# Optimization experiments

Measured on AMD Instinct MI355X. Metric: run time of the kernel, lower is better.

## Reference

```python
import jax, jax.numpy as jnp
import numpy as np

BITS = 4            # OPU.bits
VEC = 64            # OPU.input_vector_len / weight_vector_len
QMAX = 2 ** (BITS - 1) - 1   # 7


def ste_round(x):
    # straight-through round (onn_round)
    return x + jax.lax.stop_gradient(jnp.round(x) - x)


@jax.custom_vjp
def onn_dot_sum(x, w):
    # x: [N, R, VEC], w: [VEC, R, M]
    # per-chunk matmul -> clamp to int8 range -> binarize (>=0 -> 1) -> sum over chunks
    s = jnp.einsum('nrc,crm->nrm', x, w)
    s = jnp.clip(s, -128.0, 127.0)
    return jnp.where(s < 0, 0.0, 1.0).sum(axis=1)  # [N, M]


def _onn_dot_fwd(x, w):
    return onn_dot_sum(x, w), (x, w)


def _onn_dot_bwd(res, g):
    # onn_dot_fun.backward: straight-through past clamp+threshold;
    # each chunk receives the same grad g (sum over chunks).
    x, w = res
    gx = jnp.einsum('nm,crm->nrc', g, w)
    gw = jnp.einsum('nrc,nm->crm', x, g)
    return gx, gw


onn_dot_sum.defvjp(_onn_dot_fwd, _onn_dot_bwd)


def _onn_conv2d(inp, weight):
    B, C, H, W = inp.shape
    Cout, Cin, k, _ = weight.shape
    pad = (k - 1) // 2  # SAME, stride=1
    # im2col (matches torch F.unfold channel-major ordering: C, kh, kw)
    xp = jnp.pad(inp, ((0, 0), (0, 0), (pad, pad), (pad, pad)))
    patches = jnp.stack([xp[:, :, i:i + H, j:j + W]
                         for i in range(k) for j in range(k)], axis=2)  # [B,C,k*k,H,W]
    inp_unf = patches.reshape(B, C * k * k, H * W).transpose(0, 2, 1)    # [B,L,D]
    # weight quantization: STE round + clamp to 4-bit signed range
    scale = (2 ** BITS - 1) / (weight.max() - weight.min() + 1e-9)
    wq = jnp.clip(ste_round(weight * scale), -QMAX, QMAX)
    w_ = wq.reshape(Cout, -1).T                                          # [D, Cout]
    D = C * k * k
    repeats = -(-D // VEC)
    padD = VEC * repeats - D
    x = jnp.pad(inp_unf, ((0, 0), (0, 0), (0, padD))).reshape(B * H * W, repeats, VEC)
    wpad = jnp.pad(w_, ((0, padD), (0, 0)))                              # [VEC*R, Cout]
    wr = wpad.T.reshape(Cout, repeats, VEC).transpose(2, 1, 0)           # [VEC,R,Cout]
    temp = onn_dot_sum(x, wr)                                            # [B*L, Cout]
    return temp.reshape(B, H * W, Cout).transpose(0, 2, 1).reshape(B, Cout, H, W)


def setup_inputs() -> dict:
    key = jax.random.key(0)
    k1, k2 = jax.random.split(key)
    B, Cin, H, W = 16, 128, 32, 32
    Cout, k = 256, 3
    inp = jax.random.normal(k1, (B, Cin, H, W), dtype=jnp.float32)
    fan_in = Cin * k * k
    bound = 1.0 / np.sqrt(fan_in)  # kaiming_uniform with a=sqrt(5)
    weight = jax.random.uniform(k2, (Cout, Cin, k, k), dtype=jnp.float32,
                                minval=-bound, maxval=bound)
    return {"inp": inp, "weight": weight}


def reference(inp, weight):
    return _onn_conv2d(inp, weight)
```

## Files before the change

### kernel.cpp

```cpp
#include <hip/hip_runtime.h>


#define TAU 0.03f
#define HITCAP 2048

typedef short short8 __attribute__((ext_vector_type(8)));
typedef float f32x4 __attribute__((ext_vector_type(4)));
typedef unsigned int uv4 __attribute__((ext_vector_type(4)));

__device__ __forceinline__ unsigned short bf16rn(float v) {
    unsigned u = __float_as_uint(v);
    unsigned r = u + 0x7fffu + ((u >> 16) & 1u);
    return (unsigned short)(r >> 16);
}

__global__ __launch_bounds__(256) void k_prep(const float* __restrict__ w,
                                              const float* __restrict__ inp,
                                              float* __restrict__ pmin,
                                              float* __restrict__ pmax,
                                              unsigned* __restrict__ xpk) {
    if (blockIdx.x < 64) {
        int tid = blockIdx.x * 256 + threadIdx.x;
        float vmin = 1e30f, vmax = -1e30f;
        for (int i = tid; i < 294912; i += 64 * 256) {
            float v = w[i];
            vmin = fminf(vmin, v);
            vmax = fmaxf(vmax, v);
        }
        #pragma unroll
        for (int off = 32; off > 0; off >>= 1) {
            vmin = fminf(vmin, __shfl_down(vmin, off, 64));
            vmax = fmaxf(vmax, __shfl_down(vmax, off, 64));
        }
        __shared__ float smin[4], smax[4];
        int wave = threadIdx.x >> 6;
        if ((threadIdx.x & 63) == 0) { smin[wave] = vmin; smax[wave] = vmax; }
        __syncthreads();
        if (threadIdx.x == 0) {
            #pragma unroll
            for (int i = 1; i < 4; i++) {
                vmin = fminf(vmin, smin[i]);
                vmax = fmaxf(vmax, smax[i]);
            }
            pmin[blockIdx.x] = vmin;
            pmax[blockIdx.x] = vmax;
        }
    } else {
        int bc = blockIdx.x - 64;
        const float* src = inp + (size_t)bc * 1024;
        unsigned* dst = xpk + (size_t)bc * 1156;
        #pragma unroll
        for (int i = 0; i < 5; ++i) {
            int idx = threadIdx.x + i * 256;
            if (idx < 1156) {
                int yy = idx / 34, xx = idx - yy * 34;
                float v = 0.0f;
                int ys = yy - 1, xs_ = xx - 1;
                if ((unsigned)ys < 32u && (unsigned)xs_ < 32u) v = src[ys * 32 + xs_];
                unsigned short h = bf16rn(v);
                float hf = __uint_as_float((unsigned)h << 16);
                unsigned short l = bf16rn(v - hf);
                dst[idx] = (unsigned)h | ((unsigned)l << 16);
            }
        }
    }
}

__device__ __forceinline__ float block_scale(const float* pmin, const float* pmax,
                                             float* sca_lds) {
    int t = threadIdx.x;
    if (t < 64) {
        float vmin = pmin[t];
        float vmax = pmax[t];
        #pragma unroll
        for (int off = 32; off > 0; off >>= 1) {
            vmin = fminf(vmin, __shfl_down(vmin, off, 64));
            vmax = fmaxf(vmax, __shfl_down(vmax, off, 64));
        }
        if (t == 0) {
            float tt = __fadd_rn(__fsub_rn(vmax, vmin), 1e-9f);
            *sca_lds = __fdiv_rn(15.0f, tt);
        }
    }
    __syncthreads();
    return *sca_lds;
}

__global__ __launch_bounds__(256) void k_quantb(const float* __restrict__ w,
                                                const float* __restrict__ pmin,
                                                const float* __restrict__ pmax,
                                                uv4* __restrict__ wqb) {
    __shared__ float sca;
    float s = block_scale(pmin, pmax, &sca);
    int slot = blockIdx.x * 256 + threadIdx.x;
    int lane = slot & 63;
    int sub = slot >> 6;
    int khalf = sub & 1;
    int mt = (sub >> 1) & 3;
    int gr = sub >> 3;
    int g = gr / 18, r = gr - g * 18;
    int m = g * 64 + mt * 16 + (lane & 15);
    int dbase = r * 64 + khalf * 32 + (lane >> 4) * 8;
    const float* wp = w + (size_t)m * 1152 + dbase;
    unsigned o[4];
    #pragma unroll
    for (int p = 0; p < 4; ++p) {
        float q0 = rintf(__fmul_rn(wp[2 * p], s));
        float q1 = rintf(__fmul_rn(wp[2 * p + 1], s));
        q0 = fminf(fmaxf(q0, -7.0f), 7.0f);
        q1 = fminf(fmaxf(q1, -7.0f), 7.0f);
        o[p] = (unsigned)bf16rn(q0) | ((unsigned)bf16rn(q1) << 16);
    }
    uv4 v; v.x = o[0]; v.y = o[1]; v.z = o[2]; v.w = o[3];
    wqb[slot] = v;
}

#define XLD(o) (*reinterpret_cast<const unsigned*>(xpkB + (xdelta + (unsigned)(o))))

#define ISSUE_B(rr, dst) do {                                                  \
    const int4* _oa = reinterpret_cast<const int4*>(&ofs_s[(rr) * 64 + quad * 8]); \
    int4 _o0 = _oa[0], _o1 = _oa[1];                                           \
    const int4* _ob = reinterpret_cast<const int4*>(&ofs_s[(rr) * 64 + 32 + quad * 8]); \
    int4 _o2 = _ob[0], _o3 = _ob[1];                                           \
    dst[0] = XLD(_o0.x); dst[1] = XLD(_o0.y); dst[2] = XLD(_o0.z); dst[3] = XLD(_o0.w); \
    dst[4] = XLD(_o1.x); dst[5] = XLD(_o1.y); dst[6] = XLD(_o1.z); dst[7] = XLD(_o1.w); \
    dst[8] = XLD(_o2.x); dst[9] = XLD(_o2.y); dst[10] = XLD(_o2.z); dst[11] = XLD(_o2.w); \
    dst[12] = XLD(_o3.x); dst[13] = XLD(_o3.y); dst[14] = XLD(_o3.z); dst[15] = XLD(_o3.w); \
} while (0)

#define AIDX(rr, mm) ((((mm) >> 2) * 9216) + (rr) * 512 + (((mm) & 3) * 128))

__global__ __launch_bounds__(512, 4) void k_main(const unsigned* __restrict__ xpk,
                                                 const uv4* __restrict__ wqb,
                                                 const float* __restrict__ inp,
                                                 const float* __restrict__ weight,
                                                 const float* __restrict__ pmin,
                                                 const float* __restrict__ pmax,
                                                 float* __restrict__ out) {
    __shared__ alignas(16) int ofs_s[1152];
    __shared__ unsigned hitbuf[HITCAP];
    __shared__ unsigned red_s[4][64][9];
    __shared__ unsigned hitcnt;
    __shared__ float sca;

    const int t = threadIdx.x;
    if (t == 0) hitcnt = 0u;
    float sc = block_scale(pmin, pmax, &sca);
    for (int k = t; k < 1152; k += 512) {
        int cin = k / 9;
        int rem = k - cin * 9;
        int kh = rem / 3;
        int kw = rem - kh * 3;
        ofs_s[k] = (cin * 1156 + kh * 34 + kw) * 4;
    }
    __syncthreads();

    const int lane = t & 63;
    const int wv8 = t >> 6;
    const int nt = wv8 >> 1;
    const int kz = wv8 & 1;
    const int quad = lane >> 4;
    const int nl = lane & 15;
    const int n0 = blockIdx.x * 64;
    const int g = blockIdx.y;
    const int b = n0 >> 10;
    const int r0 = kz * 9, rend = r0 + 9;

    const int sy_w = ((n0 & 1023) >> 5) + (nt >> 1);
    const int col0 = (nt & 1) * 16;
    const char* __restrict__ xpkB = (const char*)xpk;
    const unsigned xdelta =
        ((unsigned)b * (128u * 1156u) + (unsigned)(sy_w * 34 + col0 + nl)) * 4u;
    const uv4* __restrict__ aw = wqb + (size_t)g * (2 * 18 * 512) + lane;

    unsigned negpk[8][2] = {};
    unsigned long long hitacc = 0ull;

    unsigned pb[16];
    ISSUE_B(r0, pb);
    short8 ac0 = __builtin_bit_cast(short8, aw[AIDX(r0, 0)]);
    short8 ac1 = __builtin_bit_cast(short8, aw[AIDX(r0, 0) + 64]);

    for (int r = r0; r < rend; ++r) {
        short8 bhi[2], blo[2];
        #pragma unroll
        for (int kh2 = 0; kh2 < 2; ++kh2) {
            union { unsigned d[4]; short8 v; } H, L;
            #pragma unroll
            for (int p = 0; p < 4; ++p) {
                unsigned ua = pb[kh2 * 8 + 2 * p], ub = pb[kh2 * 8 + 2 * p + 1];
                H.d[p] = __builtin_amdgcn_perm(ub, ua, 0x05040100u);
                L.d[p] = __builtin_amdgcn_perm(ub, ua, 0x07060302u);
            }
            bhi[kh2] = H.v;
            blo[kh2] = L.v;
        }

        const int rn = (r + 1 < rend) ? r + 1 : r;
        ISSUE_B(rn, pb);

        f32x4 accs[8];
        #pragma unroll
        for (int mt = 0; mt < 8; ++mt) {
            const int pn = (mt == 7) ? AIDX(rn, 0) : AIDX(r, mt + 1);
            short8 an0 = __builtin_bit_cast(short8, aw[pn]);
            short8 an1 = __builtin_bit_cast(short8, aw[pn + 64]);

            f32x4 acc = {0.0f, 0.0f, 0.0f, 0.0f};
            acc = __builtin_amdgcn_mfma_f32_16x16x32_bf16(ac0, bhi[0], acc, 0, 0, 0);
            acc = __builtin_amdgcn_mfma_f32_16x16x32_bf16(ac1, bhi[1], acc, 0, 0, 0);
            acc = __builtin_amdgcn_mfma_f32_16x16x32_bf16(ac0, blo[0], acc, 0, 0, 0);
            acc = __builtin_amdgcn_mfma_f32_16x16x32_bf16(ac1, blo[1], acc, 0, 0, 0);
            accs[mt] = acc;
            #pragma unroll
            for (int p = 0; p < 2; ++p) {
                unsigned sb0 = __float_as_uint(acc[2 * p]) >> 31;
                unsigned sb1 = __float_as_uint(acc[2 * p + 1]) >> 31;
                negpk[mt][p] += sb0 + (sb1 << 16);
                hitacc |= __ballot(__builtin_fabsf(acc[2 * p]) < TAU);
                hitacc |= __ballot(__builtin_fabsf(acc[2 * p + 1]) < TAU);
            }
            ac0 = an0;
            ac1 = an1;
        }

        if (hitacc) {
            #pragma unroll
            for (int mt = 0; mt < 8; ++mt)
                #pragma unroll
                for (int i = 0; i < 4; ++i) {
                    float s = accs[mt][i];
                    if (__builtin_fabsf(s) < TAU) {
                        unsigned ge = (__float_as_uint(s) >> 31) ^ 1u;
                        unsigned idx = atomicAdd(&hitcnt, 1u);
                        if (idx < (unsigned)HITCAP) {
                            unsigned m = (unsigned)(g * 128 + mt * 16 + quad * 4 + i);
                            unsigned n = (unsigned)(n0 + nt * 16 + nl);
                            hitbuf[idx] = n | ((unsigned)r << 14) | (m << 19)
                                            | (ge << 27);
                        }
                    }
                }
            hitacc = 0ull;
        }
    }

    if (kz == 1) {
        #pragma unroll
        for (int mt = 0; mt < 8; ++mt) {
            unsigned c0 = negpk[mt][0] & 0xffffu, c1 = negpk[mt][0] >> 16;
            unsigned c2 = negpk[mt][1] & 0xffffu, c3 = negpk[mt][1] >> 16;
            red_s[nt][lane][mt] = c0 | (c1 << 8) | (c2 << 16) | (c3 << 24);
        }
    }
    __syncthreads();
    if (kz == 0) {
        const int n = n0 + nt * 16 + nl;
        const int p = n & 1023;
        #pragma unroll
        for (int mt = 0; mt < 8; ++mt) {
            unsigned pk = red_s[nt][lane][mt];
            unsigned tot0 = (negpk[mt][0] & 0xffffu) + (pk & 255u);
            unsigned tot1 = (negpk[mt][0] >> 16) + ((pk >> 8) & 255u);
            unsigned tot2 = (negpk[mt][1] & 0xffffu) + ((pk >> 16) & 255u);
            unsigned tot3 = (negpk[mt][1] >> 16) + (pk >> 24);
            int mb = g * 128 + mt * 16 + quad * 4;
            size_t obase = ((size_t)(b * 256 + mb)) << 10;
            out[obase + p]              = (float)(18u - tot0);
            out[obase + (1ull << 10) + p] = (float)(18u - tot1);
            out[obase + (2ull << 10) + p] = (float)(18u - tot2);
            out[obase + (3ull << 10) + p] = (float)(18u - tot3);
        }
    }

    __syncthreads();
    unsigned tot = hitcnt;
    if (tot > (unsigned)HITCAP) tot = (unsigned)HITCAP;
    for (unsigned i = t; i < tot; i += 512) {
        unsigned u = hitbuf[i];
        int n = u & 16383;
        int r = (u >> 14) & 31;
        int m = (u >> 19) & 255;
        int bit = (u >> 27) & 1;
        int bb = n >> 10, p = n & 1023, y = p >> 5, x = p & 31;
        const float* ib = inp + (size_t)bb * (128 * 32 * 32);
        const float* wp = weight + (size_t)m * 1152;
        float s = 0.0f;
        int d = r * 64;
        for (int c = 0; c < 64; ++c, ++d) {
            int ci = d / 9, rem = d - ci * 9;
            int kh = rem / 3, kw = rem - kh * 3;
            int yy = y + kh - 1, xx = x + kw - 1;
            float xv = 0.0f;
            if ((unsigned)yy < 32u && (unsigned)xx < 32u)
                xv = ib[(ci * 32 + yy) * 32 + xx];
            float q = rintf(__fmul_rn(wp[d], sc));
            q = fminf(fmaxf(q, -7.0f), 7.0f);
            s = __fadd_rn(s, __fmul_rn(xv, q));
        }
        int nb = (s >= 0.0f) ? 1 : 0;
        if (nb != bit)
            atomicAdd(&out[(((size_t)(bb * 256 + m)) << 10) + p], nb ? 1.0f : -1.0f);
    }
}

extern "C" void kernel_launch(void* const* d_in, const int* in_sizes, int n_in,
                              void* d_out, int out_size, void* d_ws, size_t ws_size,
                              hipStream_t stream) {
    const float* inp    = (const float*)d_in[0];
    const float* weight = (const float*)d_in[1];
    float* out = (float*)d_out;

    char* ws = (char*)d_ws;
    float*    pmin  = (float*)(ws + 0);
    float*    pmax  = (float*)(ws + 256);
    uv4*      wqb   = (uv4*)(ws + 1024);
    unsigned* xpk   = (unsigned*)(ws + 590848);

    k_prep<<<2112, 256, 0, stream>>>(weight, inp, pmin, pmax, xpk);
    k_quantb<<<144, 256, 0, stream>>>(weight, pmin, pmax, wqb);

    dim3 grid(256, 2);
    k_main<<<grid, 512, 0, stream>>>(xpk, wqb, inp, weight, pmin, pmax, out);
}
```

Before: 119.3 us.

## Deepen weight-fragment prefetch to four tiles and swizzle block-to-tile mapping

Replaces the one-tile-ahead prefetch of A (weight) fragments with a four-register-set rotation, so each weight load is issued four MFMA groups before it is used. This hides more global-load latency behind matrix work. Blocks are also remapped from a linear launch index with a stride-8 swizzle, so neighbouring blocks get different n-tiles and output groups, which is meant to change cache locality and XCD distribution. The deeper prefetch holds more VGPRs live, which risks spills or lower occupancy under the 512x4 launch bounds.

```diff
diff --git a/kernel.cpp b/kernel.cpp
--- a/kernel.cpp
+++ b/kernel.cpp
@@ -130,6 +130,25 @@
 
 #define AIDX(rr, mm) ((((mm) >> 2) * 9216) + (rr) * 512 + (((mm) & 3) * 128))
 
+#define MT_STEP(mt, sA, sB, pr, pm) do {                                        \
+    f32x4 acc = {0.0f, 0.0f, 0.0f, 0.0f};                                       \
+    acc = __builtin_amdgcn_mfma_f32_16x16x32_bf16(sA, bhi[0], acc, 0, 0, 0);    \
+    acc = __builtin_amdgcn_mfma_f32_16x16x32_bf16(sB, bhi[1], acc, 0, 0, 0);    \
+    acc = __builtin_amdgcn_mfma_f32_16x16x32_bf16(sA, blo[0], acc, 0, 0, 0);    \
+    acc = __builtin_amdgcn_mfma_f32_16x16x32_bf16(sB, blo[1], acc, 0, 0, 0);    \
+    sA = __builtin_bit_cast(short8, aw[AIDX(pr, pm)]);                          \
+    sB = __builtin_bit_cast(short8, aw[AIDX(pr, pm) + 64]);                     \
+    accs[mt] = acc;                                                             \
+    _Pragma("unroll")                                                           \
+    for (int p = 0; p < 2; ++p) {                                               \
+        unsigned sb0 = __float_as_uint(acc[2 * p]) >> 31;                       \
+        unsigned sb1 = __float_as_uint(acc[2 * p + 1]) >> 31;                   \
+        negpk[mt][p] += sb0 + (sb1 << 16);                                      \
+        hitacc |= __ballot(__builtin_fabsf(acc[2 * p]) < TAU);                  \
+        hitacc |= __ballot(__builtin_fabsf(acc[2 * p + 1]) < TAU);              \
+    }                                                                           \
+} while (0)
+
 __global__ __launch_bounds__(512, 4) void k_main(const unsigned* __restrict__ xpk,
                                                  const uv4* __restrict__ wqb,
                                                  const float* __restrict__ inp,
@@ -155,14 +174,17 @@
     }
     __syncthreads();
 
+    const int lin = (int)(blockIdx.y * gridDim.x + blockIdx.x);
+    const int nlin = (lin & 7) * 64 + (lin >> 3);
+    const int g = nlin >> 8;
+    const int n0 = (nlin & 255) * 64;
+
     const int lane = t & 63;
     const int wv8 = t >> 6;
     const int nt = wv8 >> 1;
     const int kz = wv8 & 1;
     const int quad = lane >> 4;
     const int nl = lane & 15;
-    const int n0 = blockIdx.x * 64;
-    const int g = blockIdx.y;
     const int b = n0 >> 10;
     const int r0 = kz * 9, rend = r0 + 9;
 
@@ -178,8 +200,14 @@
 
     unsigned pb[16];
     ISSUE_B(r0, pb);
-    short8 ac0 = __builtin_bit_cast(short8, aw[AIDX(r0, 0)]);
-    short8 ac1 = __builtin_bit_cast(short8, aw[AIDX(r0, 0) + 64]);
+    short8 a0A = __builtin_bit_cast(short8, aw[AIDX(r0, 0)]);
+    short8 a0B = __builtin_bit_cast(short8, aw[AIDX(r0, 0) + 64]);
+    short8 a1A = __builtin_bit_cast(short8, aw[AIDX(r0, 1)]);
+    short8 a1B = __builtin_bit_cast(short8, aw[AIDX(r0, 1) + 64]);
+    short8 a2A = __builtin_bit_cast(short8, aw[AIDX(r0, 2)]);
+    short8 a2B = __builtin_bit_cast(short8, aw[AIDX(r0, 2) + 64]);
+    short8 a3A = __builtin_bit_cast(short8, aw[AIDX(r0, 3)]);
+    short8 a3B = __builtin_bit_cast(short8, aw[AIDX(r0, 3) + 64]);
 
     for (int r = r0; r < rend; ++r) {
         short8 bhi[2], blo[2];
@@ -200,29 +228,14 @@
         ISSUE_B(rn, pb);
 
         f32x4 accs[8];
-        #pragma unroll
-        for (int mt = 0; mt < 8; ++mt) {
-            const int pn = (mt == 7) ? AIDX(rn, 0) : AIDX(r, mt + 1);
-            short8 an0 = __builtin_bit_cast(short8, aw[pn]);
-            short8 an1 = __builtin_bit_cast(short8, aw[pn + 64]);
-
-            f32x4 acc = {0.0f, 0.0f, 0.0f, 0.0f};
-            acc = __builtin_amdgcn_mfma_f32_16x16x32_bf16(ac0, bhi[0], acc, 0, 0, 0);
-            acc = __builtin_amdgcn_mfma_f32_16x16x32_bf16(ac1, bhi[1], acc, 0, 0, 0);
-            acc = __builtin_amdgcn_mfma_f32_16x16x32_bf16(ac0, blo[0], acc, 0, 0, 0);
-            acc = __builtin_amdgcn_mfma_f32_16x16x32_bf16(ac1, blo[1], acc, 0, 0, 0);
-            accs[mt] = acc;
-            #pragma unroll
-            for (int p = 0; p < 2; ++p) {
-                unsigned sb0 = __float_as_uint(acc[2 * p]) >> 31;
-                unsigned sb1 = __float_as_uint(acc[2 * p + 1]) >> 31;
-                negpk[mt][p] += sb0 + (sb1 << 16);
-                hitacc |= __ballot(__builtin_fabsf(acc[2 * p]) < TAU);
-                hitacc |= __ballot(__builtin_fabsf(acc[2 * p + 1]) < TAU);
-            }
-            ac0 = an0;
-            ac1 = an1;
-        }
+        MT_STEP(0, a0A, a0B, r, 4);
+        MT_STEP(1, a1A, a1B, r, 5);
+        MT_STEP(2, a2A, a2B, r, 6);
+        MT_STEP(3, a3A, a3B, r, 7);
+        MT_STEP(4, a0A, a0B, rn, 0);
+        MT_STEP(5, a1A, a1B, rn, 1);
+        MT_STEP(6, a2A, a2B, rn, 2);
+        MT_STEP(7, a3A, a3B, rn, 3);
 
         if (hitacc) {
             #pragma unroll
@@ -266,7 +279,7 @@
             unsigned tot3 = (negpk[mt][1] >> 16) + (pk >> 24);
             int mb = g * 128 + mt * 16 + quad * 4;
             size_t obase = ((size_t)(b * 256 + mb)) << 10;
-            out[obase + p]              = (float)(18u - tot0);
+            out[obase + p]                = (float)(18u - tot0);
             out[obase + (1ull << 10) + p] = (float)(18u - tot1);
             out[obase + (2ull << 10) + p] = (float)(18u - tot2);
             out[obase + (3ull << 10) + p] = (float)(18u - tot3);
```

New measurement: 123.4 us. +3.4%, slower.

## Switch main GEMM to int8 MFMA with fixed-point split activations and prebuilt im2col

Applied to the files above, without the earlier changes.

Activations are quantized to fixed point (scale 2048) and split into hi/lo int8 halves, and the 4-bit weights are stored as int8, so the main loop uses i32 16x16x64 int8 MFMAs instead of the bf16 hi/lo decomposition. A separate k_bmat kernel materializes the im2col B-fragments in global memory, which replaces the per-lane gather through LDS offsets. The near-zero fallback threshold becomes an integer band, and the block order is swizzled for L2 locality. The cost is an extra ~37MB workspace write/read and quantization of the inputs, which relies on the exact-recompute path to correct sign flips near zero.

```diff
diff --git a/kernel.cpp b/kernel.cpp
--- a/kernel.cpp
+++ b/kernel.cpp
@@ -1,68 +1,39 @@
 #include <hip/hip_runtime.h>
 
 
-#define TAU 0.03f
-#define HITCAP 2048
-
-typedef short short8 __attribute__((ext_vector_type(8)));
-typedef float f32x4 __attribute__((ext_vector_type(4)));
+#define THRI 123
+#define HITCAP 1024
+
 typedef unsigned int uv4 __attribute__((ext_vector_type(4)));
-
-__device__ __forceinline__ unsigned short bf16rn(float v) {
-    unsigned u = __float_as_uint(v);
-    unsigned r = u + 0x7fffu + ((u >> 16) & 1u);
-    return (unsigned short)(r >> 16);
-}
+typedef int iv4 __attribute__((ext_vector_type(4)));
 
 __global__ __launch_bounds__(256) void k_prep(const float* __restrict__ w,
-                                              const float* __restrict__ inp,
                                               float* __restrict__ pmin,
-                                              float* __restrict__ pmax,
-                                              unsigned* __restrict__ xpk) {
-    if (blockIdx.x < 64) {
-        int tid = blockIdx.x * 256 + threadIdx.x;
-        float vmin = 1e30f, vmax = -1e30f;
-        for (int i = tid; i < 294912; i += 64 * 256) {
-            float v = w[i];
-            vmin = fminf(vmin, v);
-            vmax = fmaxf(vmax, v);
-        }
-        #pragma unroll
-        for (int off = 32; off > 0; off >>= 1) {
-            vmin = fminf(vmin, __shfl_down(vmin, off, 64));
-            vmax = fmaxf(vmax, __shfl_down(vmax, off, 64));
-        }
-        __shared__ float smin[4], smax[4];
-        int wave = threadIdx.x >> 6;
-        if ((threadIdx.x & 63) == 0) { smin[wave] = vmin; smax[wave] = vmax; }
-        __syncthreads();
-        if (threadIdx.x == 0) {
-            #pragma unroll
-            for (int i = 1; i < 4; i++) {
-                vmin = fminf(vmin, smin[i]);
-                vmax = fmaxf(vmax, smax[i]);
-            }
-            pmin[blockIdx.x] = vmin;
-            pmax[blockIdx.x] = vmax;
-        }
-    } else {
-        int bc = blockIdx.x - 64;
-        const float* src = inp + (size_t)bc * 1024;
-        unsigned* dst = xpk + (size_t)bc * 1156;
-        #pragma unroll
-        for (int i = 0; i < 5; ++i) {
-            int idx = threadIdx.x + i * 256;
-            if (idx < 1156) {
-                int yy = idx / 34, xx = idx - yy * 34;
-                float v = 0.0f;
-                int ys = yy - 1, xs_ = xx - 1;
-                if ((unsigned)ys < 32u && (unsigned)xs_ < 32u) v = src[ys * 32 + xs_];
-                unsigned short h = bf16rn(v);
-                float hf = __uint_as_float((unsigned)h << 16);
-                unsigned short l = bf16rn(v - hf);
-                dst[idx] = (unsigned)h | ((unsigned)l << 16);
-            }
-        }
+                                              float* __restrict__ pmax) {
+    int tid = blockIdx.x * 256 + threadIdx.x;
+    float vmin = 1e30f, vmax = -1e30f;
+    for (int i = tid; i < 294912; i += 64 * 256) {
+        float v = w[i];
+        vmin = fminf(vmin, v);
+        vmax = fmaxf(vmax, v);
+    }
+    #pragma unroll
+    for (int off = 32; off > 0; off >>= 1) {
+        vmin = fminf(vmin, __shfl_down(vmin, off, 64));
+        vmax = fmaxf(vmax, __shfl_down(vmax, off, 64));
+    }
+    __shared__ float smin[4], smax[4];
+    int wave = threadIdx.x >> 6;
+    if ((threadIdx.x & 63) == 0) { smin[wave] = vmin; smax[wave] = vmax; }
+    __syncthreads();
+    if (threadIdx.x == 0) {
+        #pragma unroll
+        for (int i = 1; i < 4; i++) {
+            vmin = fminf(vmin, smin[i]);
+            vmax = fmaxf(vmax, smax[i]);
+        }
+        pmin[blockIdx.x] = vmin;
+        pmax[blockIdx.x] = vmax;
     }
 }
 
@@ -86,58 +57,73 @@
     return *sca_lds;
 }
 
+__global__ __launch_bounds__(256) void k_bmat(const float* __restrict__ inp,
+                                              uv4* __restrict__ bmh,
+                                              uv4* __restrict__ bml) {
+    const int t = threadIdx.x;
+    const int lane = t & 63;
+    const int unit = blockIdx.x * 4 + (t >> 6);
+    const int r = unit >> 10;
+    const int n16 = unit & 1023;
+    const int nl = lane & 15, kq = lane >> 4;
+    const int n = n16 * 16 + nl;
+    const int b = n >> 10, p = n & 1023, y = p >> 5, x = p & 31;
+    const float* ib = inp + ((size_t)b << 17);
+    unsigned hw[4] = {0u, 0u, 0u, 0u}, lw[4] = {0u, 0u, 0u, 0u};
+    #pragma unroll
+    for (int j = 0; j < 16; ++j) {
+        int d = r * 64 + kq * 16 + j;
+        int ci = d / 9, rem = d - ci * 9;
+        int kh = rem / 3, kw = rem - kh * 3;
+        int yy = y + kh - 1, xx = x + kw - 1;
+        float v = 0.0f;
+        if ((unsigned)yy < 32u && (unsigned)xx < 32u)
+            v = ib[(ci << 10) + yy * 32 + xx];
+        int xq = (int)rintf(v * 2048.0f);
+        int hi = (xq + 64) >> 7;
+        int lo = xq - (hi << 7);
+        hw[j >> 2] |= ((unsigned)hi & 255u) << ((j & 3) * 8);
+        lw[j >> 2] |= ((unsigned)lo & 255u) << ((j & 3) * 8);
+    }
+    int slot = unit * 64 + lane;
+    uv4 hv; hv.x = hw[0]; hv.y = hw[1]; hv.z = hw[2]; hv.w = hw[3];
+    uv4 lv; lv.x = lw[0]; lv.y = lw[1]; lv.z = lw[2]; lv.w = lw[3];
+    bmh[slot] = hv;
+    bml[slot] = lv;
+}
+
 __global__ __launch_bounds__(256) void k_quantb(const float* __restrict__ w,
                                                 const float* __restrict__ pmin,
                                                 const float* __restrict__ pmax,
-                                                uv4* __restrict__ wqb) {
+                                                uv4* __restrict__ aq) {
     __shared__ float sca;
     float s = block_scale(pmin, pmax, &sca);
     int slot = blockIdx.x * 256 + threadIdx.x;
     int lane = slot & 63;
     int sub = slot >> 6;
-    int khalf = sub & 1;
-    int mt = (sub >> 1) & 3;
-    int gr = sub >> 3;
-    int g = gr / 18, r = gr - g * 18;
-    int m = g * 64 + mt * 16 + (lane & 15);
-    int dbase = r * 64 + khalf * 32 + (lane >> 4) * 8;
+    int mtg = sub & 15, r = sub >> 4;
+    int m = mtg * 16 + (lane & 15);
+    int dbase = r * 64 + (lane >> 4) * 16;
     const float* wp = w + (size_t)m * 1152 + dbase;
-    unsigned o[4];
+    unsigned wv_[4] = {0u, 0u, 0u, 0u};
     #pragma unroll
-    for (int p = 0; p < 4; ++p) {
-        float q0 = rintf(__fmul_rn(wp[2 * p], s));
-        float q1 = rintf(__fmul_rn(wp[2 * p + 1], s));
-        q0 = fminf(fmaxf(q0, -7.0f), 7.0f);
-        q1 = fminf(fmaxf(q1, -7.0f), 7.0f);
-        o[p] = (unsigned)bf16rn(q0) | ((unsigned)bf16rn(q1) << 16);
-    }
-    uv4 v; v.x = o[0]; v.y = o[1]; v.z = o[2]; v.w = o[3];
-    wqb[slot] = v;
-}
-
-#define XLD(o) (*reinterpret_cast<const unsigned*>(xpkB + (xdelta + (unsigned)(o))))
-
-#define ISSUE_B(rr, dst) do {                                                  \
-    const int4* _oa = reinterpret_cast<const int4*>(&ofs_s[(rr) * 64 + quad * 8]); \
-    int4 _o0 = _oa[0], _o1 = _oa[1];                                           \
-    const int4* _ob = reinterpret_cast<const int4*>(&ofs_s[(rr) * 64 + 32 + quad * 8]); \
-    int4 _o2 = _ob[0], _o3 = _ob[1];                                           \
-    dst[0] = XLD(_o0.x); dst[1] = XLD(_o0.y); dst[2] = XLD(_o0.z); dst[3] = XLD(_o0.w); \
-    dst[4] = XLD(_o1.x); dst[5] = XLD(_o1.y); dst[6] = XLD(_o1.z); dst[7] = XLD(_o1.w); \
-    dst[8] = XLD(_o2.x); dst[9] = XLD(_o2.y); dst[10] = XLD(_o2.z); dst[11] = XLD(_o2.w); \
-    dst[12] = XLD(_o3.x); dst[13] = XLD(_o3.y); dst[14] = XLD(_o3.z); dst[15] = XLD(_o3.w); \
-} while (0)
-
-#define AIDX(rr, mm) ((((mm) >> 2) * 9216) + (rr) * 512 + (((mm) & 3) * 128))
-
-__global__ __launch_bounds__(512, 4) void k_main(const unsigned* __restrict__ xpk,
-                                                 const uv4* __restrict__ wqb,
+    for (int j = 0; j < 16; ++j) {
+        float q = rintf(__fmul_rn(wp[j], s));
+        q = fminf(fmaxf(q, -7.0f), 7.0f);
+        wv_[j >> 2] |= ((unsigned)(int)q & 255u) << ((j & 3) * 8);
+    }
+    uv4 v; v.x = wv_[0]; v.y = wv_[1]; v.z = wv_[2]; v.w = wv_[3];
+    aq[slot] = v;
+}
+
+__global__ __launch_bounds__(512, 4) void k_main(const uv4* __restrict__ aq,
+                                                 const uv4* __restrict__ bmh,
+                                                 const uv4* __restrict__ bml,
                                                  const float* __restrict__ inp,
                                                  const float* __restrict__ weight,
                                                  const float* __restrict__ pmin,
                                                  const float* __restrict__ pmax,
                                                  float* __restrict__ out) {
-    __shared__ alignas(16) int ofs_s[1152];
     __shared__ unsigned hitbuf[HITCAP];
     __shared__ unsigned red_s[4][64][9];
     __shared__ unsigned hitcnt;
@@ -146,14 +132,11 @@
     const int t = threadIdx.x;
     if (t == 0) hitcnt = 0u;
     float sc = block_scale(pmin, pmax, &sca);
-    for (int k = t; k < 1152; k += 512) {
-        int cin = k / 9;
-        int rem = k - cin * 9;
-        int kh = rem / 3;
-        int kw = rem - kh * 3;
-        ofs_s[k] = (cin * 1156 + kh * 34 + kw) * 4;
-    }
-    __syncthreads();
+
+    const int lin = (int)(blockIdx.y * gridDim.x + blockIdx.x);
+    const int nlin = (lin & 7) * 64 + (lin >> 3);
+    const int g = nlin >> 8;
+    const int n0 = (nlin & 255) * 64;
 
     const int lane = t & 63;
     const int wv8 = t >> 6;
@@ -161,67 +144,46 @@
     const int kz = wv8 & 1;
     const int quad = lane >> 4;
     const int nl = lane & 15;
-    const int n0 = blockIdx.x * 64;
-    const int g = blockIdx.y;
     const int b = n0 >> 10;
     const int r0 = kz * 9, rend = r0 + 9;
 
-    const int sy_w = ((n0 & 1023) >> 5) + (nt >> 1);
-    const int col0 = (nt & 1) * 16;
-    const char* __restrict__ xpkB = (const char*)xpk;
-    const unsigned xdelta =
-        ((unsigned)b * (128u * 1156u) + (unsigned)(sy_w * 34 + col0 + nl)) * 4u;
-    const uv4* __restrict__ aw = wqb + (size_t)g * (2 * 18 * 512) + lane;
+    const int n16g = (n0 >> 4) + nt;
+    const int sb = n16g * 64 + lane;
+    const uv4* __restrict__ awq = aq + lane;
 
     unsigned negpk[8][2] = {};
     unsigned long long hitacc = 0ull;
 
-    unsigned pb[16];
-    ISSUE_B(r0, pb);
-    short8 ac0 = __builtin_bit_cast(short8, aw[AIDX(r0, 0)]);
-    short8 ac1 = __builtin_bit_cast(short8, aw[AIDX(r0, 0) + 64]);
+    uv4 pbh = bmh[r0 * 65536 + sb];
+    uv4 pbl = bml[r0 * 65536 + sb];
 
     for (int r = r0; r < rend; ++r) {
-        short8 bhi[2], blo[2];
-        #pragma unroll
-        for (int kh2 = 0; kh2 < 2; ++kh2) {
-            union { unsigned d[4]; short8 v; } H, L;
+        iv4 bhv = __builtin_bit_cast(iv4, pbh);
+        iv4 blv = __builtin_bit_cast(iv4, pbl);
+
+        const int rn = (r + 1 < rend) ? r + 1 : r;
+        pbh = bmh[rn * 65536 + sb];
+        pbl = bml[rn * 65536 + sb];
+
+        iv4 accs[8];
+        #pragma unroll
+        for (int mt = 0; mt < 8; ++mt) {
+            iv4 av = __builtin_bit_cast(iv4, awq[(r * 16 + g * 8 + mt) * 64]);
+            iv4 z = {0, 0, 0, 0};
+            iv4 ah = __builtin_amdgcn_mfma_i32_16x16x64_i8(av, bhv, z, 0, 0, 0);
+            iv4 al = __builtin_amdgcn_mfma_i32_16x16x64_i8(av, blv, z, 0, 0, 0);
+            iv4 s;
             #pragma unroll
-            for (int p = 0; p < 4; ++p) {
-                unsigned ua = pb[kh2 * 8 + 2 * p], ub = pb[kh2 * 8 + 2 * p + 1];
-                H.d[p] = __builtin_amdgcn_perm(ub, ua, 0x05040100u);
-                L.d[p] = __builtin_amdgcn_perm(ub, ua, 0x07060302u);
-            }
-            bhi[kh2] = H.v;
-            blo[kh2] = L.v;
-        }
-
-        const int rn = (r + 1 < rend) ? r + 1 : r;
-        ISSUE_B(rn, pb);
-
-        f32x4 accs[8];
-        #pragma unroll
-        for (int mt = 0; mt < 8; ++mt) {
-            const int pn = (mt == 7) ? AIDX(rn, 0) : AIDX(r, mt + 1);
-            short8 an0 = __builtin_bit_cast(short8, aw[pn]);
-            short8 an1 = __builtin_bit_cast(short8, aw[pn + 64]);
-
-            f32x4 acc = {0.0f, 0.0f, 0.0f, 0.0f};
-            acc = __builtin_amdgcn_mfma_f32_16x16x32_bf16(ac0, bhi[0], acc, 0, 0, 0);
-            acc = __builtin_amdgcn_mfma_f32_16x16x32_bf16(ac1, bhi[1], acc, 0, 0, 0);
-            acc = __builtin_amdgcn_mfma_f32_16x16x32_bf16(ac0, blo[0], acc, 0, 0, 0);
-            acc = __builtin_amdgcn_mfma_f32_16x16x32_bf16(ac1, blo[1], acc, 0, 0, 0);
-            accs[mt] = acc;
+            for (int i = 0; i < 4; ++i) s[i] = (ah[i] << 7) + al[i];
+            accs[mt] = s;
             #pragma unroll
             for (int p = 0; p < 2; ++p) {
-                unsigned sb0 = __float_as_uint(acc[2 * p]) >> 31;
-                unsigned sb1 = __float_as_uint(acc[2 * p + 1]) >> 31;
+                unsigned sb0 = (unsigned)s[2 * p] >> 31;
+                unsigned sb1 = (unsigned)s[2 * p + 1] >> 31;
                 negpk[mt][p] += sb0 + (sb1 << 16);
-                hitacc |= __ballot(__builtin_fabsf(acc[2 * p]) < TAU);
-                hitacc |= __ballot(__builtin_fabsf(acc[2 * p + 1]) < TAU);
+                hitacc |= __ballot((unsigned)(s[2 * p] + (THRI - 1)) < (unsigned)(2 * THRI - 1));
+                hitacc |= __ballot((unsigned)(s[2 * p + 1] + (THRI - 1)) < (unsigned)(2 * THRI - 1));
             }
-            ac0 = an0;
-            ac1 = an1;
         }
 
         if (hitacc) {
@@ -229,9 +191,9 @@
             for (int mt = 0; mt < 8; ++mt)
                 #pragma unroll
                 for (int i = 0; i < 4; ++i) {
-                    float s = accs[mt][i];
-                    if (__builtin_fabsf(s) < TAU) {
-                        unsigned ge = (__float_as_uint(s) >> 31) ^ 1u;
+                    int s = accs[mt][i];
+                    if ((unsigned)(s + (THRI - 1)) < (unsigned)(2 * THRI - 1)) {
+                        unsigned ge = ((unsigned)s >> 31) ^ 1u;
                         unsigned idx = atomicAdd(&hitcnt, 1u);
                         if (idx < (unsigned)HITCAP) {
                             unsigned m = (unsigned)(g * 128 + mt * 16 + quad * 4 + i);
@@ -266,7 +228,7 @@
             unsigned tot3 = (negpk[mt][1] >> 16) + (pk >> 24);
             int mb = g * 128 + mt * 16 + quad * 4;
             size_t obase = ((size_t)(b * 256 + mb)) << 10;
-            out[obase + p]              = (float)(18u - tot0);
+            out[obase + p]                = (float)(18u - tot0);
             out[obase + (1ull << 10) + p] = (float)(18u - tot1);
             out[obase + (2ull << 10) + p] = (float)(18u - tot2);
             out[obase + (3ull << 10) + p] = (float)(18u - tot3);
@@ -312,14 +274,16 @@
     float* out = (float*)d_out;
 
     char* ws = (char*)d_ws;
-    float*    pmin  = (float*)(ws + 0);
-    float*    pmax  = (float*)(ws + 256);
-    uv4*      wqb   = (uv4*)(ws + 1024);
-    unsigned* xpk   = (unsigned*)(ws + 590848);
-
-    k_prep<<<2112, 256, 0, stream>>>(weight, inp, pmin, pmax, xpk);
-    k_quantb<<<144, 256, 0, stream>>>(weight, pmin, pmax, wqb);
+    float* pmin = (float*)(ws + 0);
+    float* pmax = (float*)(ws + 256);
+    uv4*   aq   = (uv4*)(ws + 1024);
+    uv4*   bmh  = (uv4*)(ws + 296960);
+    uv4*   bml  = (uv4*)(ws + 19171328);
+
+    k_prep<<<64, 256, 0, stream>>>(weight, pmin, pmax);
+    k_bmat<<<4608, 256, 0, stream>>>(inp, bmh, bml);
+    k_quantb<<<72, 256, 0, stream>>>(weight, pmin, pmax, aq);
 
     dim3 grid(256, 2);
-    k_main<<<grid, 512, 0, stream>>>(xpk, wqb, inp, weight, pmin, pmax, out);
-}
+    k_main<<<grid, 512, 0, stream>>>(aq, bmh, bml, inp, weight, pmin, pmax, out);
+}
```

New measurement: 148.9 us. 24.8% more time.

## Fuse weight min/max and quantization into prep kernel; swizzle main grid

Applied to the files above, without the earlier changes.

Merges the weight min/max reduction and the weight quantization into the input-packing kernel, so one launch replaces two. Each of the 144 quantization blocks now recomputes the full weight min/max itself with float4 loads, which removes the partial-reduction buffers. The main kernel reads a single precomputed scale instead of reducing 64 partials in every block. It also remaps block indices so that consecutive blocks interleave across both output-channel groups and spatial tiles. The cost is redundant reading of the whole weight tensor by every quantization block.

```diff
diff --git a/kernel.cpp b/kernel.cpp
--- a/kernel.cpp
+++ b/kernel.cpp
@@ -16,42 +16,17 @@
 
 __global__ __launch_bounds__(256) void k_prep(const float* __restrict__ w,
                                               const float* __restrict__ inp,
-                                              float* __restrict__ pmin,
-                                              float* __restrict__ pmax,
-                                              unsigned* __restrict__ xpk) {
-    if (blockIdx.x < 64) {
-        int tid = blockIdx.x * 256 + threadIdx.x;
-        float vmin = 1e30f, vmax = -1e30f;
-        for (int i = tid; i < 294912; i += 64 * 256) {
-            float v = w[i];
-            vmin = fminf(vmin, v);
-            vmax = fmaxf(vmax, v);
-        }
-        #pragma unroll
-        for (int off = 32; off > 0; off >>= 1) {
-            vmin = fminf(vmin, __shfl_down(vmin, off, 64));
-            vmax = fmaxf(vmax, __shfl_down(vmax, off, 64));
-        }
-        __shared__ float smin[4], smax[4];
-        int wave = threadIdx.x >> 6;
-        if ((threadIdx.x & 63) == 0) { smin[wave] = vmin; smax[wave] = vmax; }
-        __syncthreads();
-        if (threadIdx.x == 0) {
-            #pragma unroll
-            for (int i = 1; i < 4; i++) {
-                vmin = fminf(vmin, smin[i]);
-                vmax = fmaxf(vmax, smax[i]);
-            }
-            pmin[blockIdx.x] = vmin;
-            pmax[blockIdx.x] = vmax;
-        }
-    } else {
-        int bc = blockIdx.x - 64;
+                                              unsigned* __restrict__ xpk,
+                                              uv4* __restrict__ wqb,
+                                              float* __restrict__ wsscale) {
+    const int t = threadIdx.x;
+    if (blockIdx.x < 2048) {
+        int bc = blockIdx.x;
         const float* src = inp + (size_t)bc * 1024;
         unsigned* dst = xpk + (size_t)bc * 1156;
         #pragma unroll
         for (int i = 0; i < 5; ++i) {
-            int idx = threadIdx.x + i * 256;
+            int idx = t + i * 256;
             if (idx < 1156) {
                 int yy = idx / 34, xx = idx - yy * 34;
                 float v = 0.0f;
@@ -63,56 +38,59 @@
                 dst[idx] = (unsigned)h | ((unsigned)l << 16);
             }
         }
-    }
-}
-
-__device__ __forceinline__ float block_scale(const float* pmin, const float* pmax,
-                                             float* sca_lds) {
-    int t = threadIdx.x;
-    if (t < 64) {
-        float vmin = pmin[t];
-        float vmax = pmax[t];
+    } else {
+        const float4* w4 = (const float4*)w;
+        float vmin = 1e30f, vmax = -1e30f;
+        for (int i = t; i < 73728; i += 256) {
+            float4 v = w4[i];
+            vmin = fminf(vmin, fminf(fminf(v.x, v.y), fminf(v.z, v.w)));
+            vmax = fmaxf(vmax, fmaxf(fmaxf(v.x, v.y), fmaxf(v.z, v.w)));
+        }
         #pragma unroll
         for (int off = 32; off > 0; off >>= 1) {
             vmin = fminf(vmin, __shfl_down(vmin, off, 64));
             vmax = fmaxf(vmax, __shfl_down(vmax, off, 64));
         }
+        __shared__ float smin[4], smax[4];
+        __shared__ float sca;
+        int wave = t >> 6;
+        if ((t & 63) == 0) { smin[wave] = vmin; smax[wave] = vmax; }
+        __syncthreads();
         if (t == 0) {
+            #pragma unroll
+            for (int i = 1; i < 4; i++) {
+                vmin = fminf(vmin, smin[i]);
+                vmax = fmaxf(vmax, smax[i]);
+            }
             float tt = __fadd_rn(__fsub_rn(vmax, vmin), 1e-9f);
-            *sca_lds = __fdiv_rn(15.0f, tt);
-        }
-    }
-    __syncthreads();
-    return *sca_lds;
-}
-
-__global__ __launch_bounds__(256) void k_quantb(const float* __restrict__ w,
-                                                const float* __restrict__ pmin,
-                                                const float* __restrict__ pmax,
-                                                uv4* __restrict__ wqb) {
-    __shared__ float sca;
-    float s = block_scale(pmin, pmax, &sca);
-    int slot = blockIdx.x * 256 + threadIdx.x;
-    int lane = slot & 63;
-    int sub = slot >> 6;
-    int khalf = sub & 1;
-    int mt = (sub >> 1) & 3;
-    int gr = sub >> 3;
-    int g = gr / 18, r = gr - g * 18;
-    int m = g * 64 + mt * 16 + (lane & 15);
-    int dbase = r * 64 + khalf * 32 + (lane >> 4) * 8;
-    const float* wp = w + (size_t)m * 1152 + dbase;
-    unsigned o[4];
-    #pragma unroll
-    for (int p = 0; p < 4; ++p) {
-        float q0 = rintf(__fmul_rn(wp[2 * p], s));
-        float q1 = rintf(__fmul_rn(wp[2 * p + 1], s));
-        q0 = fminf(fmaxf(q0, -7.0f), 7.0f);
-        q1 = fminf(fmaxf(q1, -7.0f), 7.0f);
-        o[p] = (unsigned)bf16rn(q0) | ((unsigned)bf16rn(q1) << 16);
-    }
-    uv4 v; v.x = o[0]; v.y = o[1]; v.z = o[2]; v.w = o[3];
-    wqb[slot] = v;
+            sca = __fdiv_rn(15.0f, tt);
+            wsscale[0] = sca;
+        }
+        __syncthreads();
+        float s = sca;
+
+        int slot = (int)(blockIdx.x - 2048) * 256 + t;
+        int lane = slot & 63;
+        int sub = slot >> 6;
+        int khalf = sub & 1;
+        int mt = (sub >> 1) & 3;
+        int gr = sub >> 3;
+        int g = gr / 18, r = gr - g * 18;
+        int m = g * 64 + mt * 16 + (lane & 15);
+        int dbase = r * 64 + khalf * 32 + (lane >> 4) * 8;
+        const float* wp = w + (size_t)m * 1152 + dbase;
+        unsigned o[4];
+        #pragma unroll
+        for (int p = 0; p < 4; ++p) {
+            float q0 = rintf(__fmul_rn(wp[2 * p], s));
+            float q1 = rintf(__fmul_rn(wp[2 * p + 1], s));
+            q0 = fminf(fmaxf(q0, -7.0f), 7.0f);
+            q1 = fminf(fmaxf(q1, -7.0f), 7.0f);
+            o[p] = (unsigned)bf16rn(q0) | ((unsigned)bf16rn(q1) << 16);
+        }
+        uv4 v; v.x = o[0]; v.y = o[1]; v.z = o[2]; v.w = o[3];
+        wqb[slot] = v;
+    }
 }
 
 #define XLD(o) (*reinterpret_cast<const unsigned*>(xpkB + (xdelta + (unsigned)(o))))
@@ -134,18 +112,16 @@
                                                  const uv4* __restrict__ wqb,
                                                  const float* __restrict__ inp,
                                                  const float* __restrict__ weight,
-                                                 const float* __restrict__ pmin,
-                                                 const float* __restrict__ pmax,
+                                                 const float* __restrict__ wsscale,
                                                  float* __restrict__ out) {
     __shared__ alignas(16) int ofs_s[1152];
     __shared__ unsigned hitbuf[HITCAP];
     __shared__ unsigned red_s[4][64][9];
     __shared__ unsigned hitcnt;
-    __shared__ float sca;
 
     const int t = threadIdx.x;
     if (t == 0) hitcnt = 0u;
-    float sc = block_scale(pmin, pmax, &sca);
+    const float sc = wsscale[0];
     for (int k = t; k < 1152; k += 512) {
         int cin = k / 9;
         int rem = k - cin * 9;
@@ -155,14 +131,17 @@
     }
     __syncthreads();
 
+    const int lin = (int)(blockIdx.y * gridDim.x + blockIdx.x);
+    const int nlin = (lin & 7) * 64 + (lin >> 3);
+    const int g = nlin >> 8;
+    const int n0 = (nlin & 255) * 64;
+
     const int lane = t & 63;
     const int wv8 = t >> 6;
     const int nt = wv8 >> 1;
     const int kz = wv8 & 1;
     const int quad = lane >> 4;
     const int nl = lane & 15;
-    const int n0 = blockIdx.x * 64;
-    const int g = blockIdx.y;
     const int b = n0 >> 10;
     const int r0 = kz * 9, rend = r0 + 9;
 
@@ -266,7 +245,7 @@
             unsigned tot3 = (negpk[mt][1] >> 16) + (pk >> 24);
             int mb = g * 128 + mt * 16 + quad * 4;
             size_t obase = ((size_t)(b * 256 + mb)) << 10;
-            out[obase + p]              = (float)(18u - tot0);
+            out[obase + p]                = (float)(18u - tot0);
             out[obase + (1ull << 10) + p] = (float)(18u - tot1);
             out[obase + (2ull << 10) + p] = (float)(18u - tot2);
             out[obase + (3ull << 10) + p] = (float)(18u - tot3);
@@ -312,14 +291,12 @@
     float* out = (float*)d_out;
 
     char* ws = (char*)d_ws;
-    float*    pmin  = (float*)(ws + 0);
-    float*    pmax  = (float*)(ws + 256);
-    uv4*      wqb   = (uv4*)(ws + 1024);
-    unsigned* xpk   = (unsigned*)(ws + 590848);
-
-    k_prep<<<2112, 256, 0, stream>>>(weight, inp, pmin, pmax, xpk);
-    k_quantb<<<144, 256, 0, stream>>>(weight, pmin, pmax, wqb);
+    float*    wsscale = (float*)(ws + 0);
+    uv4*      wqb     = (uv4*)(ws + 1024);
+    unsigned* xpk     = (unsigned*)(ws + 590848);
+
+    k_prep<<<2192, 256, 0, stream>>>(weight, inp, xpk, wqb, wsscale);
 
     dim3 grid(256, 2);
-    k_main<<<grid, 512, 0, stream>>>(xpk, wqb, inp, weight, pmin, pmax, out);
+    k_main<<<grid, 512, 0, stream>>>(xpk, wqb, inp, weight, wsscale, out);
 }
```

New measurement: 190.4 us. 59.6% more time.
